# Kernel optimization log

Hardware: AMD Instinct MI355X
Metric: run time of the kernel (lower is better)

Reference implementation:

```python
import jax, jax.numpy as jnp
import numpy as np

D_MODEL = 1024
N_HEADS = 16
D_K = D_MODEL // N_HEADS
D_FF = 4096
EPS = 1e-5


def setup_inputs() -> dict:
    key = jax.random.key(0)
    ks = jax.random.split(key, 16)
    s = 0.02
    d, f = D_MODEL, D_FF
    return {
        'ebd_x': jax.random.normal(ks[0], (2, 2048, d), jnp.float32),
        'Wq': jax.random.normal(ks[1], (d, d), jnp.float32) * s,
        'bq': jnp.zeros((d,), jnp.float32),
        'Wk': jax.random.normal(ks[2], (d, d), jnp.float32) * s,
        'bk': jnp.zeros((d,), jnp.float32),
        'Wv': jax.random.normal(ks[3], (d, d), jnp.float32) * s,
        'bv': jnp.zeros((d,), jnp.float32),
        'Wo': jax.random.normal(ks[4], (d, d), jnp.float32) * s,
        'bo': jnp.zeros((d,), jnp.float32),
        'W1': jax.random.normal(ks[5], (d, f), jnp.float32) * s,
        'b1': jnp.zeros((f,), jnp.float32),
        'W2': jax.random.normal(ks[6], (f, d), jnp.float32) * s,
        'b2': jnp.zeros((d,), jnp.float32),
        'g1': jnp.ones((d,), jnp.float32),
        'beta1': jnp.zeros((d,), jnp.float32),
        'g2': jnp.ones((d,), jnp.float32),
        'beta2': jnp.zeros((d,), jnp.float32),
    }


def _layernorm(x, g, b):
    mu = jnp.mean(x, axis=-1, keepdims=True)
    var = jnp.mean(jnp.square(x - mu), axis=-1, keepdims=True)
    return (x - mu) * jax.lax.rsqrt(var + EPS) * g + b


def reference(ebd_x, Wq, bq, Wk, bk, Wv, bv, Wo, bo, W1, b1, W2, b2, g1, beta1, g2, beta2):
    b, L, d = ebd_x.shape
    h, dk = N_HEADS, D_K
    # QKV projections, split heads: (b, h, L, dk)
    q = (ebd_x @ Wq + bq).reshape(b, L, h, dk).transpose(0, 2, 1, 3)
    k = (ebd_x @ Wk + bk).reshape(b, L, h, dk).transpose(0, 2, 1, 3)
    v = (ebd_x @ Wv + bv).reshape(b, L, h, dk).transpose(0, 2, 1, 3)
    scores = jnp.einsum('bhLd,bhld->bhLl', q, k) / jnp.sqrt(jnp.float32(dk))
    attn = jax.nn.softmax(scores, axis=-1)
    attn_v = jnp.einsum('bhLl,bhld->bhLd', attn, v)
    # faithful to source: reshape (b,h,L,dk) -> (b,L,d) WITHOUT transposing back
    attn_v = attn_v.reshape(b, L, d)
    attn_v = attn_v @ Wo + bo
    # dropout is identity in eval mode
    x1 = _layernorm(attn_v + ebd_x, g1, beta1)
    ff = jax.nn.gelu(x1 @ W1 + b1, approximate=False) @ W2 + b2
    return _layernorm(ff + x1, g2, beta2)
```

## Files before the change

kernel.cpp:

```cpp
#include <hip/hip_runtime.h>
#include <hip/hip_bf16.h>
#include <math.h>

typedef __bf16 bhalf;
typedef __bf16 bhalf8 __attribute__((ext_vector_type(8)));
typedef float  floatx4 __attribute__((ext_vector_type(4)));
typedef float  floatx8 __attribute__((ext_vector_type(8)));
typedef unsigned short ushort_t;
typedef unsigned short ushort8 __attribute__((ext_vector_type(8)));

#define MFMA16(a, b, c) __builtin_amdgcn_mfma_f32_16x16x32_bf16((a), (b), (c), 0, 0, 0)

__device__ __forceinline__ void gload_lds16(const bhalf* g, bhalf* l)
{
    __builtin_amdgcn_global_load_lds((const __attribute__((address_space(1))) void*)g,
                                     (__attribute__((address_space(3))) void*)l, 16, 0, 0);
}

enum { EPI_PLAIN = 0, EPI_RES = 1, EPI_GELU = 2, EPI_QKV = 3 };

__global__ __launch_bounds__(256) void detect_dtype(const ushort_t* __restrict__ x,
                                                    int* __restrict__ flag)
{
    __shared__ int tot;
    if (threadIdx.x == 0) tot = 0;
    __syncthreads();
    int cnt = 0;
#pragma unroll
    for (int it = 0; it < 8; ++it) {
        const ushort8 u = *(const ushort8*)(x + ((size_t)(it * 256 + threadIdx.x)) * 8);
#pragma unroll
        for (int j = 0; j < 8; j += 2) {
            const int e = (u[j] >> 7) & 0xFF;
            if (e >= 0x90) ++cnt;
        }
    }
    atomicAdd(&tot, cnt);
    __syncthreads();
    if (threadIdx.x == 0) flag[0] = (tot > 64) ? 1 : 0;
}

__global__ __launch_bounds__(256) void norm_x(const void* __restrict__ s,
                                              bhalf* __restrict__ d,
                                              const int* __restrict__ flag)
{
    const int i = (blockIdx.x * 256 + threadIdx.x) * 8;
    if (*flag) {
        const floatx8 v = *(const floatx8*)((const float*)s + i);
        bhalf8 o;
#pragma unroll
        for (int j = 0; j < 8; ++j) o[j] = (bhalf)v[j];
        *(bhalf8*)(d + i) = o;
    } else {
        *(ushort8*)((ushort_t*)d + i) = *(const ushort8*)((const ushort_t*)s + i);
    }
}

struct Cvt { const void* s; bhalf* d; int n; };
struct CvtArr { Cvt t[10]; };

__global__ __launch_bounds__(256) void norm_vec(CvtArr a, const int* __restrict__ flag)
{
    const Cvt c = a.t[blockIdx.y];
    const int i = (blockIdx.x * 256 + threadIdx.x) * 8;
    if (i >= c.n) return;
    if (*flag) {
        const floatx8 v = *(const floatx8*)((const float*)c.s + i);
        bhalf8 o;
#pragma unroll
        for (int j = 0; j < 8; ++j) o[j] = (bhalf)v[j];
        *(bhalf8*)(c.d + i) = o;
    } else {
        *(ushort8*)((ushort_t*)c.d + i) = *(const ushort8*)((const ushort_t*)c.s + i);
    }
}

struct TDesc { const void* src; bhalf* dst; int R, C; };
struct TDescArr { TDesc t[6]; };

__global__ __launch_bounds__(256) void transpose_all(TDescArr a, const int* __restrict__ flag)
{
    __shared__ bhalf sm[32][33];
    const int id = blockIdx.x;
    TDesc d;
    int rem;
    if (id < 4096)      { d = a.t[id >> 10]; rem = id & 1023; }
    else if (id < 8192) { d = a.t[4];        rem = id - 4096; }
    else                { d = a.t[5];        rem = id - 8192; }
    const int txc = d.C >> 5;
    const int bx = (rem % txc) * 32;
    const int by = (rem / txc) * 32;
    const int tx = threadIdx.x & 31;
    const int ty = threadIdx.x >> 5;
    if (*flag) {
        const float* fin = (const float*)d.src;
#pragma unroll
        for (int i = 0; i < 4; ++i)
            sm[ty + i * 8][tx] = (bhalf)fin[(size_t)(by + ty + i * 8) * d.C + bx + tx];
    } else {
        const bhalf* bin = (const bhalf*)d.src;
#pragma unroll
        for (int i = 0; i < 4; ++i)
            sm[ty + i * 8][tx] = bin[(size_t)(by + ty + i * 8) * d.C + bx + tx];
    }
    __syncthreads();
#pragma unroll
    for (int i = 0; i < 4; ++i)
        d.dst[(size_t)(bx + ty + i * 8) * d.R + by + tx] = sm[tx][ty + i * 8];
}

__global__ __launch_bounds__(256) void vt_transpose(const bhalf* __restrict__ Vw,
                                                    bhalf* __restrict__ Vt)
{
    __shared__ bhalf sm[32][33];
    const int bh = blockIdx.z;
    const int b = bh >> 4, h = bh & 15;
    const int tb = blockIdx.y * 32;
    const int db = blockIdx.x * 32;
    const int tx = threadIdx.x & 31;
    const int ty = threadIdx.x >> 5;
#pragma unroll
    for (int i = 0; i < 4; ++i)
        sm[ty + i * 8][tx] = Vw[(size_t)(b * 2048 + tb + ty + i * 8) * 1024 + h * 64 + db + tx];
    __syncthreads();
#pragma unroll
    for (int i = 0; i < 4; ++i)
        Vt[(size_t)(bh * 64 + db + ty + i * 8) * 2048 + tb + tx] = sm[tx][ty + i * 8];
}

template <int EPI, int TN>
__global__ __launch_bounds__(256) void gemm128(
    const bhalf* __restrict__ A, int lda,
    const bhalf* __restrict__ BT, int ldb,
    const bhalf* __restrict__ bias,
    const bhalf* __restrict__ resid,
    bhalf* __restrict__ C, int ldc, int K,
    bhalf* __restrict__ Ck, bhalf* __restrict__ Cv)
{
    __shared__ __align__(16) bhalf As[128 * 64];
    __shared__ __align__(16) bhalf Bs[TN * 64];

    const int tid  = threadIdx.x;
    const int lane = tid & 63;
    const int w    = tid >> 6;
    const int l15  = lane & 15;
    const int q    = lane >> 4;
    constexpr int MT = (TN == 128) ? 4 : 2;
    const int wm   = (TN == 128) ? (w >> 1) * 64 : w * 32;
    const int wn   = (TN == 128) ? (w & 1) * 64 : 0;
    const int n0   = blockIdx.x * TN;
    const int m0   = blockIdx.y * 128;

    const int r8 = lane >> 3;
    const int c8 = lane & 7;
    const int gc = (c8 ^ r8) << 3;

    floatx4 acc[MT][4];
#pragma unroll
    for (int i = 0; i < MT; ++i)
#pragma unroll
        for (int j = 0; j < 4; ++j) acc[i][j] = (floatx4){0.f, 0.f, 0.f, 0.f};

    for (int k0 = 0; k0 < K; k0 += 64) {
        __syncthreads();
#pragma unroll
        for (int i = 0; i < 4; ++i) {
            const int rb = w * 32 + i * 8;
            gload_lds16(A + (size_t)(m0 + rb + r8) * lda + k0 + gc, &As[rb * 64] + lane * 8);
        }
        if constexpr (TN == 128) {
#pragma unroll
            for (int i = 0; i < 4; ++i) {
                const int rb = w * 32 + i * 8;
                gload_lds16(BT + (size_t)(n0 + rb + r8) * ldb + k0 + gc, &Bs[rb * 64] + lane * 8);
            }
        } else {
#pragma unroll
            for (int i = 0; i < 2; ++i) {
                const int rb = w * 16 + i * 8;
                gload_lds16(BT + (size_t)(n0 + rb + r8) * ldb + k0 + gc, &Bs[rb * 64] + lane * 8);
            }
        }
        __syncthreads();
#pragma unroll
        for (int s = 0; s < 2; ++s) {
            const int pc = (((s * 4 + q) ^ (l15 & 7)) << 3);
            bhalf8 af[MT], bf[4];
#pragma unroll
            for (int mt = 0; mt < MT; ++mt)
                af[mt] = *(const bhalf8*)&As[(wm + mt * 16 + l15) * 64 + pc];
#pragma unroll
            for (int nt = 0; nt < 4; ++nt)
                bf[nt] = *(const bhalf8*)&Bs[(wn + nt * 16 + l15) * 64 + pc];
#pragma unroll
            for (int mt = 0; mt < MT; ++mt)
#pragma unroll
                for (int nt = 0; nt < 4; ++nt)
                    acc[mt][nt] = MFMA16(af[mt], bf[nt], acc[mt][nt]);
        }
    }

#pragma unroll
    for (int mt = 0; mt < MT; ++mt)
#pragma unroll
        for (int nt = 0; nt < 4; ++nt) {
            const int col = n0 + wn + nt * 16 + l15;
            const float bv = (float)bias[col];
#pragma unroll
            for (int r = 0; r < 4; ++r) {
                const int row = m0 + wm + mt * 16 + q * 4 + r;
                float v = acc[mt][nt][r] + bv;
                if constexpr (EPI == EPI_PLAIN) {
                    C[(size_t)row * ldc + col] = (bhalf)v;
                } else if constexpr (EPI == EPI_RES) {
                    v += (float)resid[(size_t)row * ldc + col];
                    C[(size_t)row * ldc + col] = (bhalf)v;
                } else if constexpr (EPI == EPI_GELU) {
                    v = 0.5f * v * (1.f + erff(v * 0.70710678118654752f));
                    C[(size_t)row * ldc + col] = (bhalf)v;
                } else {
                    if (col < 1024)       C [(size_t)row * 1024 + col]        = (bhalf)v;
                    else if (col < 2048)  Ck[(size_t)row * 1024 + col - 1024] = (bhalf)v;
                    else                  Cv[(size_t)row * 1024 + col - 2048] = (bhalf)v;
                }
            }
        }
}

__global__ __launch_bounds__(256) void flash_attn(
    const bhalf* __restrict__ Q, const bhalf* __restrict__ Km,
    const bhalf* __restrict__ Vt, bhalf* __restrict__ ctx)
{
    __shared__ __align__(16) bhalf Ks[2][64 * 64];
    __shared__ __align__(16) bhalf Vs[2][64 * 64];
    __shared__ __align__(16) bhalf Ps[64 * 64];

    const int tid  = threadIdx.x;
    const int lane = tid & 63;
    const int wq   = tid >> 6;
    const int l15  = lane & 15;
    const int q    = lane >> 4;
    const int bh   = blockIdx.x & 31;
    const int l0   = (blockIdx.x >> 5) * 64;
    const int b    = bh >> 4, h = bh & 15;
    const float SC = 0.125f * 1.44269504f;

    const bhalf* qp = Q + ((size_t)(b * 2048 + l0 + wq * 16 + l15)) * 1024 + h * 64 + q * 8;
    const bhalf8 aQ0 = *(const bhalf8*)qp;
    const bhalf8 aQ1 = *(const bhalf8*)(qp + 32);

    float ps[4] = {0.f, 0.f, 0.f, 0.f};
    floatx4 o[4];
#pragma unroll
    for (int ot = 0; ot < 4; ++ot) o[ot] = (floatx4){0.f, 0.f, 0.f, 0.f};

    const int r8 = lane >> 3;
    const int c8 = lane & 7;
    const int gc = (c8 ^ r8) << 3;
    const bhalf* kbase = Km + ((size_t)(b * 2048)) * 1024 + h * 64;
    const bhalf* vbase = Vt + ((size_t)(bh * 64)) * 2048;

    auto stage = [&](int buf, int kt) {
#pragma unroll
        for (int i = 0; i < 2; ++i) {
            const int rb = wq * 16 + i * 8;
            gload_lds16(kbase + (size_t)(kt + rb + r8) * 1024 + gc, &Ks[buf][rb * 64] + lane * 8);
            gload_lds16(vbase + (size_t)(rb + r8) * 2048 + kt + gc, &Vs[buf][rb * 64] + lane * 8);
        }
    };

    stage(0, 0);
    int cur = 0;
    for (int kt = 0; kt < 2048; kt += 64) {
        __syncthreads();
        if (kt + 64 < 2048) stage(cur ^ 1, kt + 64);

        floatx4 s[4];
#pragma unroll
        for (int nt = 0; nt < 4; ++nt) {
            s[nt] = (floatx4){0.f, 0.f, 0.f, 0.f};
            bhalf8 bK0 = *(const bhalf8*)&Ks[cur][(nt * 16 + l15) * 64 + ((q ^ (l15 & 7)) << 3)];
            bhalf8 bK1 = *(const bhalf8*)&Ks[cur][(nt * 16 + l15) * 64 + (((4 + q) ^ (l15 & 7)) << 3)];
            s[nt] = MFMA16(aQ0, bK0, s[nt]);
            s[nt] = MFMA16(aQ1, bK1, s[nt]);
        }
#pragma unroll
        for (int nt = 0; nt < 4; ++nt)
#pragma unroll
            for (int r = 0; r < 4; ++r) {
                const float pv = __builtin_amdgcn_exp2f(fmaf(s[nt][r], SC, -8.f));
                ps[r] += pv;
                const int row = wq * 16 + q * 4 + r;
                const int pc = (2 * nt + (l15 >> 3)) ^ ((q * 4 + r) & 7);
                Ps[row * 64 + pc * 8 + (l15 & 7)] = (bhalf)pv;
            }

#pragma unroll
        for (int kc = 0; kc < 2; ++kc) {
            bhalf8 aP = *(const bhalf8*)&Ps[(wq * 16 + l15) * 64 + (((kc * 4 + q) ^ (l15 & 7)) << 3)];
#pragma unroll
            for (int ot = 0; ot < 4; ++ot) {
                bhalf8 bV = *(const bhalf8*)&Vs[cur][(ot * 16 + l15) * 64 + (((kc * 4 + q) ^ (l15 & 7)) << 3)];
                o[ot] = MFMA16(aP, bV, o[ot]);
            }
        }
        cur ^= 1;
    }

    float inv[4];
#pragma unroll
    for (int r = 0; r < 4; ++r) {
#pragma unroll
        for (int off = 1; off < 16; off <<= 1) ps[r] += __shfl_xor(ps[r], off);
        inv[r] = 1.f / ps[r];
    }
#pragma unroll
    for (int ot = 0; ot < 4; ++ot)
#pragma unroll
        for (int r = 0; r < 4; ++r) {
            const int l = l0 + wq * 16 + q * 4 + r;
            const int kk = ot * 16 + l15;
            const int R = h * 128 + (l >> 4);
            const int Cc = (l & 15) * 64 + kk;
            ctx[((size_t)(b * 2048 + R)) * 1024 + Cc] = (bhalf)(o[ot][r] * inv[r]);
        }
}

__global__ __launch_bounds__(256) void ln_kernel(
    const bhalf* __restrict__ X, const bhalf* __restrict__ g,
    const bhalf* __restrict__ be, void* __restrict__ out, const int* __restrict__ flag)
{
    __shared__ float red[4][2];
    const int tid = threadIdx.x;
    const int wid = tid >> 6;
    const int rid = tid >> 7;
    const int lt  = tid & 127;
    const int row = blockIdx.x * 2 + rid;
    const int col = lt * 8;
    const bhalf8 xv = *(const bhalf8*)(X + (size_t)row * 1024 + col);
    float v[8], s1 = 0.f, s2 = 0.f;
#pragma unroll
    for (int i = 0; i < 8; ++i) {
        v[i] = (float)xv[i];
        s1 += v[i];
        s2 += v[i] * v[i];
    }
#pragma unroll
    for (int off = 1; off < 64; off <<= 1) {
        s1 += __shfl_xor(s1, off);
        s2 += __shfl_xor(s2, off);
    }
    if ((tid & 63) == 0) { red[wid][0] = s1; red[wid][1] = s2; }
    __syncthreads();
    const float t1 = red[rid * 2][0] + red[rid * 2 + 1][0];
    const float t2 = red[rid * 2][1] + red[rid * 2 + 1][1];
    const float mu = t1 * (1.f / 1024.f);
    const float rs = rsqrtf(t2 * (1.f / 1024.f) - mu * mu + 1e-5f);
    const bool f32 = flag && (*flag != 0);
    if (f32) {
        floatx8 ov;
#pragma unroll
        for (int i = 0; i < 8; ++i)
            ov[i] = ((v[i] - mu) * rs) * (float)g[col + i] + (float)be[col + i];
        *(floatx8*)((float*)out + (size_t)row * 1024 + col) = ov;
    } else {
        bhalf8 ov;
#pragma unroll
        for (int i = 0; i < 8; ++i)
            ov[i] = (bhalf)(((v[i] - mu) * rs) * (float)g[col + i] + (float)be[col + i]);
        *(bhalf8*)((bhalf*)out + (size_t)row * 1024 + col) = ov;
    }
}

extern "C" void kernel_launch(void* const* d_in, const int* in_sizes, int n_in,
                              void* d_out, int out_size, void* d_ws, size_t ws_size,
                              hipStream_t stream)
{
    (void)in_sizes; (void)n_in; (void)out_size; (void)ws_size;

    char* p = (char*)d_ws;
    const size_t MB = 1024 * 1024;
    int*   flag  = (int*)p;
    bhalf* vecs  = (bhalf*)(p + 128 * 1024);
    bhalf* Qw    = (bhalf*)(p + 1 * MB);
    bhalf* Kw    = (bhalf*)(p + 9 * MB);
    bhalf* Vw    = (bhalf*)(p + 17 * MB);
    bhalf* Vt    = (bhalf*)(p + 25 * MB);
    bhalf* x_n   = (bhalf*)(p + 33 * MB);
    bhalf* WqkvT = (bhalf*)(p + 41 * MB);
    bhalf* WoT   = (bhalf*)(p + 47 * MB);
    bhalf* W1T   = (bhalf*)(p + 49 * MB);
    bhalf* W2T   = (bhalf*)(p + 57 * MB);
    bhalf* ctx   = Vw;
    bhalf* ff1   = (bhalf*)(p + 17 * MB);
    bhalf* ln1   = Qw;
    bhalf* x1    = Kw;
    bhalf* ff2   = Qw;

    bhalf* bqkv  = vecs;
    bhalf* bo_n  = vecs + 1 * 4096;
    bhalf* b1_n  = vecs + 2 * 4096;
    bhalf* b2_n  = vecs + 3 * 4096;
    bhalf* g1_n  = vecs + 4 * 4096;
    bhalf* be1_n = vecs + 5 * 4096;
    bhalf* g2_n  = vecs + 6 * 4096;
    bhalf* be2_n = vecs + 7 * 4096;

    const dim3 blk(256);

    detect_dtype<<<1, blk, 0, stream>>>((const ushort_t*)d_in[0], flag);

    norm_x<<<2048, blk, 0, stream>>>(d_in[0], x_n, flag);
    CvtArr arr;
    arr.t[0] = {d_in[2],  bqkv,        1024};
    arr.t[1] = {d_in[4],  bqkv + 1024, 1024};
    arr.t[2] = {d_in[6],  bqkv + 2048, 1024};
    arr.t[3] = {d_in[8],  bo_n,        1024};
    arr.t[4] = {d_in[10], b1_n,        4096};
    arr.t[5] = {d_in[12], b2_n,        1024};
    arr.t[6] = {d_in[13], g1_n,        1024};
    arr.t[7] = {d_in[14], be1_n,       1024};
    arr.t[8] = {d_in[15], g2_n,        1024};
    arr.t[9] = {d_in[16], be2_n,       1024};
    norm_vec<<<dim3(2, 10), blk, 0, stream>>>(arr, flag);

    TDescArr td;
    td.t[0] = {d_in[1],  WqkvT,               1024, 1024};
    td.t[1] = {d_in[3],  WqkvT + 1024 * 1024, 1024, 1024};
    td.t[2] = {d_in[5],  WqkvT + 2048 * 1024, 1024, 1024};
    td.t[3] = {d_in[7],  WoT,                 1024, 1024};
    td.t[4] = {d_in[9],  W1T,                 1024, 4096};
    td.t[5] = {d_in[11], W2T,                 4096, 1024};
    transpose_all<<<12288, blk, 0, stream>>>(td, flag);

    gemm128<EPI_QKV, 128><<<dim3(24, 32), blk, 0, stream>>>(
        x_n, 1024, WqkvT, 1024, bqkv, nullptr, Qw, 1024, 1024, Kw, Vw);

    vt_transpose<<<dim3(2, 64, 32), blk, 0, stream>>>(Vw, Vt);

    flash_attn<<<1024, blk, 0, stream>>>(Qw, Kw, Vt, ctx);

    gemm128<EPI_RES, 64><<<dim3(16, 32), blk, 0, stream>>>(
        ctx, 1024, WoT, 1024, bo_n, x_n, ln1, 1024, 1024, nullptr, nullptr);
    ln_kernel<<<2048, blk, 0, stream>>>(ln1, g1_n, be1_n, x1, nullptr);

    gemm128<EPI_GELU, 128><<<dim3(32, 32), blk, 0, stream>>>(
        x1, 1024, W1T, 1024, b1_n, nullptr, ff1, 4096, 1024, nullptr, nullptr);
    gemm128<EPI_RES, 64><<<dim3(16, 32), blk, 0, stream>>>(
        ff1, 4096, W2T, 4096, b2_n, x1, ff2, 1024, 4096, nullptr, nullptr);
    ln_kernel<<<2048, blk, 0, stream>>>(ff2, g2_n, be2_n, d_out, flag);
}
```

Baseline: 393.2 us.

## Compute S transposed so P stays in registers, dropping the LDS round-trip

```diff
diff --git a/kernel.cpp b/kernel.cpp
--- a/kernel.cpp
+++ b/kernel.cpp
@@ -233,7 +233,6 @@
 {
     __shared__ __align__(16) bhalf Ks[2][64 * 64];
     __shared__ __align__(16) bhalf Vs[2][64 * 64];
-    __shared__ __align__(16) bhalf Ps[64 * 64];
 
     const int tid  = threadIdx.x;
     const int lane = tid & 63;
@@ -249,14 +248,13 @@
     const bhalf8 aQ0 = *(const bhalf8*)qp;
     const bhalf8 aQ1 = *(const bhalf8*)(qp + 32);
 
-    float ps[4] = {0.f, 0.f, 0.f, 0.f};
+    float ps = 0.f;
     floatx4 o[4];
 #pragma unroll
     for (int ot = 0; ot < 4; ++ot) o[ot] = (floatx4){0.f, 0.f, 0.f, 0.f};
 
     const int r8 = lane >> 3;
     const int c8 = lane & 7;
-    const int gc = (c8 ^ r8) << 3;
     const bhalf* kbase = Km + ((size_t)(b * 2048)) * 1024 + h * 64;
     const bhalf* vbase = Vt + ((size_t)(bh * 64)) * 2048;
 
@@ -264,8 +262,11 @@
 #pragma unroll
         for (int i = 0; i < 2; ++i) {
             const int rb = wq * 16 + i * 8;
-            gload_lds16(kbase + (size_t)(kt + rb + r8) * 1024 + gc, &Ks[buf][rb * 64] + lane * 8);
-            gload_lds16(vbase + (size_t)(rb + r8) * 2048 + kt + gc, &Vs[buf][rb * 64] + lane * 8);
+            const int fk = (((rb >> 3) << 1) ^ r8) & 7;
+            gload_lds16(kbase + (size_t)(kt + rb + r8) * 1024 + ((c8 ^ fk) << 3),
+                        &Ks[buf][rb * 64] + lane * 8);
+            gload_lds16(vbase + (size_t)(rb + r8) * 2048 + kt + ((c8 ^ r8) << 3),
+                        &Vs[buf][rb * 64] + lane * 8);
         }
     };
 
@@ -278,42 +279,43 @@
         floatx4 s[4];
 #pragma unroll
         for (int nt = 0; nt < 4; ++nt) {
-            s[nt] = (floatx4){0.f, 0.f, 0.f, 0.f};
-            bhalf8 bK0 = *(const bhalf8*)&Ks[cur][(nt * 16 + l15) * 64 + ((q ^ (l15 & 7)) << 3)];
-            bhalf8 bK1 = *(const bhalf8*)&Ks[cur][(nt * 16 + l15) * 64 + (((4 + q) ^ (l15 & 7)) << 3)];
-            s[nt] = MFMA16(aQ0, bK0, s[nt]);
-            s[nt] = MFMA16(aQ1, bK1, s[nt]);
-        }
+            const int row = (nt >> 1) * 32 + (nt & 1) * 4 + ((l15 >> 2) << 3) + (l15 & 3);
+            const int f = (((row >> 3) << 1) ^ row) & 7;
+            const bhalf8 k0 = *(const bhalf8*)&Ks[cur][row * 64 + ((q ^ f) << 3)];
+            const bhalf8 k1 = *(const bhalf8*)&Ks[cur][row * 64 + (((4 + q) ^ f) << 3)];
+            floatx4 z = (floatx4){0.f, 0.f, 0.f, 0.f};
+            z = MFMA16(k0, aQ0, z);
+            s[nt] = MFMA16(k1, aQ1, z);
+        }
+
+        bhalf8 pa[2];
 #pragma unroll
         for (int nt = 0; nt < 4; ++nt)
 #pragma unroll
             for (int r = 0; r < 4; ++r) {
                 const float pv = __builtin_amdgcn_exp2f(fmaf(s[nt][r], SC, -8.f));
-                ps[r] += pv;
-                const int row = wq * 16 + q * 4 + r;
-                const int pc = (2 * nt + (l15 >> 3)) ^ ((q * 4 + r) & 7);
-                Ps[row * 64 + pc * 8 + (l15 & 7)] = (bhalf)pv;
+                ps += pv;
+                pa[nt >> 1][(nt & 1) * 4 + r] = (bhalf)pv;
             }
 
 #pragma unroll
-        for (int kc = 0; kc < 2; ++kc) {
-            bhalf8 aP = *(const bhalf8*)&Ps[(wq * 16 + l15) * 64 + (((kc * 4 + q) ^ (l15 & 7)) << 3)];
+        for (int kc = 0; kc < 2; ++kc)
 #pragma unroll
             for (int ot = 0; ot < 4; ++ot) {
-                bhalf8 bV = *(const bhalf8*)&Vs[cur][(ot * 16 + l15) * 64 + (((kc * 4 + q) ^ (l15 & 7)) << 3)];
-                o[ot] = MFMA16(aP, bV, o[ot]);
+                const bhalf8 bV = *(const bhalf8*)&Vs[cur][(ot * 16 + l15) * 64 + (((kc * 4 + q) ^ (l15 & 7)) << 3)];
+                o[ot] = MFMA16(pa[kc], bV, o[ot]);
             }
-        }
         cur ^= 1;
     }
 
+    ps += __shfl_xor(ps, 16);
+    ps += __shfl_xor(ps, 32);
+    const float invq = 1.f / ps;
     float inv[4];
 #pragma unroll
-    for (int r = 0; r < 4; ++r) {
-#pragma unroll
-        for (int off = 1; off < 16; off <<= 1) ps[r] += __shfl_xor(ps[r], off);
-        inv[r] = 1.f / ps[r];
-    }
+    for (int r = 0; r < 4; ++r)
+        inv[r] = __shfl(invq, (lane & 48) | (q * 4 + r));
+
 #pragma unroll
     for (int ot = 0; ot < 4; ++ot)
 #pragma unroll
```

Measured after the change: 381.8 us. -2.9%, faster.
